# Performance work log

Measured on AMD Instinct MI355X. Metric: run time of the kernel, lower is better.

## Reference

```python
import jax, jax.numpy as jnp
import numpy as np
import math

D_MODEL = 1024
D_STATE = 64
DT_MIN, DT_MAX = 1e-3, 1e-1


def setup_inputs() -> dict:
    key = jax.random.key(0)
    ks = jax.random.split(key, 8)
    x = jax.random.normal(ks[0], (2, 4096, D_MODEL), dtype=jnp.float32)
    # in_proj / out_proj: nn.Linear default init (kaiming-uniform-ish); uniform is fine for a reference
    lim = 1.0 / math.sqrt(D_MODEL)
    Win = jax.random.uniform(ks[1], (D_MODEL, D_MODEL), minval=-lim, maxval=lim, dtype=jnp.float32)
    bin_ = jax.random.uniform(ks[2], (D_MODEL,), minval=-lim, maxval=lim, dtype=jnp.float32)
    Wout = jax.random.uniform(ks[3], (D_MODEL, D_MODEL), minval=-lim, maxval=lim, dtype=jnp.float32)
    bout = jax.random.uniform(ks[4], (D_MODEL,), minval=-lim, maxval=lim, dtype=jnp.float32)
    # HiPPO-LegS style init: A_log[d, n] = log(n + 1)
    A_log = jnp.broadcast_to(jnp.log(jnp.arange(1, D_STATE + 1, dtype=jnp.float32)), (D_MODEL, D_STATE))
    B = 0.1 * jax.random.normal(ks[5], (D_MODEL, D_STATE), dtype=jnp.float32)
    C = 0.1 * jax.random.normal(ks[6], (D_MODEL, D_STATE), dtype=jnp.float32)
    Dp = jnp.ones((D_MODEL,), dtype=jnp.float32)
    log_dt = jax.random.uniform(ks[7], (D_MODEL,), dtype=jnp.float32) * (math.log(DT_MAX) - math.log(DT_MIN)) + math.log(DT_MIN)
    dt = jnp.exp(log_dt)
    return {"x": x, "Win": Win, "bin_": bin_, "A_log": A_log, "B": B, "C": C,
            "Dp": Dp, "dt": dt, "Wout": Wout, "bout": bout}


def reference(x, Win, bin_, A_log, B, C, Dp, dt, Wout, bout):
    b, L, d = x.shape
    x = x @ Win.T + bin_                      # in_proj
    u = jnp.transpose(x, (0, 2, 1))           # [b, d, l]
    A = -jnp.exp(-A_log)                      # [d, n], negative real poles
    logdA = A * dt[:, None]                   # log(dA) since dA = exp(A*dt) > 0
    dB = B * dt[:, None]                      # [d, n]
    t = jnp.arange(L, dtype=x.dtype)
    # dA**t == exp(t * log dA): vectorized Vandermonde, replaces per-step power loop
    powers = jnp.exp(logdA[:, :, None] * t)   # [d, n, L]
    k = jnp.einsum('dn,dnl->dl', C * dB, powers)  # SSM conv kernel [d, L]
    n_fft = 2 * L
    k_f = jnp.fft.rfft(k, n=n_fft)            # [d, F]
    u_f = jnp.fft.rfft(u, n=n_fft)            # [b, d, F]
    y = jnp.fft.irfft(u_f * k_f[None], n=n_fft)[..., :L]  # causal conv
    y = y + u * Dp[:, None]                   # skip connection
    y = jnp.transpose(y, (0, 2, 1))           # [b, l, d]
    return y @ Wout.T + bout                  # out_proj
```

## Files before the change

### kernel.cpp

```cpp
#include <hip/hip_runtime.h>
#include <cstdint>
#include <cstddef>

#define D_MODEL 1024
#define D_STATE 64
#define SEQ     4096
#define BATCH   2
#define MROWS   (BATCH*SEQ)

typedef __bf16 bf16x8 __attribute__((ext_vector_type(8)));
typedef float  f32x4  __attribute__((ext_vector_type(4)));
typedef unsigned short u16;
typedef unsigned int   u32;

union BF8 { bf16x8 v; uint4 q; u16 e[8]; };

__device__ __forceinline__ u16 f2bf(float x) {
    u32 u = __float_as_uint(x);
    u32 r = u + 0x7FFFu + ((u >> 16) & 1u);
    return (u16)(r >> 16);
}
__device__ __forceinline__ float bf2f(u16 h) {
    return __uint_as_float(((u32)h) << 16);
}
__device__ __forceinline__ uint4 pack8u(const u16* e) {
    return make_uint4((u32)e[0] | ((u32)e[1] << 16), (u32)e[2] | ((u32)e[3] << 16),
                      (u32)e[4] | ((u32)e[5] << 16), (u32)e[6] | ((u32)e[7] << 16));
}

__device__ __forceinline__ void async16(const void* g, void* l) {
    __builtin_amdgcn_global_load_lds(
        (const __attribute__((address_space(1))) unsigned int*)(uintptr_t)g,
        (__attribute__((address_space(3))) unsigned int*)(uintptr_t)l,
        16, 0, 0);
}

__global__ __launch_bounds__(256) void prep_kernel(
    const float* __restrict__ x, const float* __restrict__ Win,
    const float* __restrict__ Wout,
    u16* __restrict__ Ax, u16* __restrict__ Bw1, u16* __restrict__ Bw2)
{
    const int blk = blockIdx.x, tid = threadIdx.x;
    const int k = tid * 4;
    const float* src; u16* dst; int row;
    if (blk < MROWS)                  { src = x;    dst = Ax;  row = blk; }
    else if (blk < MROWS + D_MODEL)   { src = Win;  dst = Bw1; row = blk - MROWS; }
    else                              { src = Wout; dst = Bw2; row = blk - MROWS - D_MODEL; }
    const float4 v = *reinterpret_cast<const float4*>(src + (size_t)row * D_MODEL + k);
    *reinterpret_cast<uint2*>(dst + (size_t)row * D_MODEL + k) =
        make_uint2((u32)f2bf(v.x) | ((u32)f2bf(v.y) << 16),
                   (u32)f2bf(v.z) | ((u32)f2bf(v.w) << 16));
}

template<int MODE>
__global__ __launch_bounds__(256) void gemm_bt(
    const u16* __restrict__ A, const u16* __restrict__ Bm,
    const float* __restrict__ bias, float* __restrict__ out)
{
    __shared__ u16 As[128 * 64];
    __shared__ u16 Bs[128 * 64];
    const int m0 = blockIdx.y * 128, n0 = blockIdx.x * 128;
    const int tid = threadIdx.x;
    const int wave = tid >> 6, lane = tid & 63;
    const int wm = wave >> 1, wn = wave & 1;
    const int qm = lane & 15, qk = lane >> 4;
    f32x4 acc[4][4] = {};
    for (int k0 = 0; k0 < D_MODEL; k0 += 64) {
        #pragma unroll
        for (int it = 0; it < 4; ++it) {
            const int c   = it * 256 + tid;
            const int row = c >> 3, col = (c & 7) * 8;
            const int ldsbase = (it * 256 + wave * 64) * 8;
            async16(&A[(size_t)(m0 + row) * D_MODEL + k0 + col], &As[ldsbase]);
            async16(&Bm[(size_t)(n0 + row) * D_MODEL + k0 + col], &Bs[ldsbase]);
        }
        __syncthreads();
        #pragma unroll
        for (int kk = 0; kk < 2; ++kk) {
            bf16x8 af[4], bg[4];
            #pragma unroll
            for (int i = 0; i < 4; ++i) {
                af[i] = *reinterpret_cast<const bf16x8*>(&As[(wm*64 + i*16 + qm)*64 + kk*32 + qk*8]);
                bg[i] = *reinterpret_cast<const bf16x8*>(&Bs[(wn*64 + i*16 + qm)*64 + kk*32 + qk*8]);
            }
            #pragma unroll
            for (int i = 0; i < 4; ++i)
                #pragma unroll
                for (int j = 0; j < 4; ++j)
                    acc[i][j] = __builtin_amdgcn_mfma_f32_16x16x32_bf16(af[i], bg[j], acc[i][j], 0, 0, 0);
        }
        __syncthreads();
    }
    #pragma unroll
    for (int i = 0; i < 4; ++i) {
        const int r0 = m0 + wm*64 + i*16 + qk*4;
        #pragma unroll
        for (int j = 0; j < 4; ++j) {
            const int c = n0 + wn*64 + j*16 + qm;
            const float bv = bias[c];
            if (MODE == 0) {
                #pragma unroll
                for (int reg = 0; reg < 4; ++reg)
                    out[(size_t)(r0 + reg) * D_MODEL + c] = acc[i][j][reg] + bv;
            } else {
                const int bb = r0 >> 12;
                const int l  = r0 & (SEQ - 1);
                float4 v = make_float4(acc[i][j][0] + bv, acc[i][j][1] + bv,
                                       acc[i][j][2] + bv, acc[i][j][3] + bv);
                *reinterpret_cast<float4*>(&out[((size_t)(bb * D_MODEL + c)) * SEQ + l]) = v;
            }
        }
    }
}

__global__ __launch_bounds__(64) void prep2_kernel(
    const float* __restrict__ A_log, const float* __restrict__ Bp,
    const float* __restrict__ Cp, const float* __restrict__ dtp,
    u16* __restrict__ Tg)
{
    __shared__ float P[64 * 65];
    __shared__ float k_sh[64];
    const int d = blockIdx.x, lane = threadIdx.x;
    const float dt_d  = dtp[d];
    const float logdA = -expf(-A_log[d * D_STATE + lane]) * dt_d;
    const float r     = expf(logdA);
    const float dBn   = Bp[d * D_STATE + lane] * dt_d;
    const float Cv    = Cp[d * D_STATE + lane];
    u16* tg = Tg + (size_t)d * 12288;

    {
        float p = Cv;
        for (int t = 0; t < 64; ++t) { p *= r; P[t * 65 + lane] = p; }
    }
    __syncthreads();
    {
        const int t = lane;
        for (int o = 0; o < 8; ++o) {
            u16 e[8];
            #pragma unroll
            for (int i = 0; i < 8; ++i) e[i] = f2bf(P[t * 65 + o * 8 + i]);
            *reinterpret_cast<uint4*>(&tg[8192 + t * 64 + o * 8]) = pack8u(e);
        }
    }
    __syncthreads();
    {
        float p = Cv * dBn;
        for (int m = 0; m < 64; ++m) { P[m * 65 + lane] = p; p *= r; }
    }
    __syncthreads();
    {
        float kacc = 0.f;
        for (int n = 0; n < 64; ++n) kacc += P[lane * 65 + n];
        k_sh[lane] = kacc;
    }
    __syncthreads();
    {
        const int t = lane;
        for (int o = 0; o < 8; ++o) {
            u16 e[8];
            #pragma unroll
            for (int i = 0; i < 8; ++i) {
                const int j = o * 8 + i;
                e[i] = (j <= t) ? f2bf(k_sh[t - j]) : (u16)0;
            }
            *reinterpret_cast<uint4*>(&tg[t * 64 + o * 8]) = pack8u(e);
        }
    }
    {
        for (int o = 0; o < 8; ++o) {
            float tmp[8];
            tmp[7] = expf(logdA * (float)(63 - (o * 8 + 7)));
            #pragma unroll
            for (int i = 6; i >= 0; --i) tmp[i] = tmp[i + 1] * r;
            u16 e[8];
            #pragma unroll
            for (int i = 0; i < 8; ++i) e[i] = f2bf(tmp[i]);
            *reinterpret_cast<uint4*>(&tg[4096 + lane * 64 + o * 8]) = pack8u(e);
        }
    }
}

__global__ __launch_bounds__(128) void scan2_kernel(
    float* __restrict__ ut, const float* __restrict__ A_log,
    const float* __restrict__ Bp, const float* __restrict__ dtp,
    const float* __restrict__ Dpv, const u16* __restrict__ Tg)
{
    __shared__ u16 KT_s[64 * 72];
    __shared__ u16 RA_s[64 * 72];
    __shared__ u16 P2_s[64 * 72];
    __shared__ u16 SH[2][64 * 72];
    const int d = blockIdx.x, tid = threadIdx.x;
    const int w = tid >> 6, lane = tid & 63;
    const int qm = lane & 15, qk = lane >> 4;

    const u16* tg = Tg + (size_t)d * 12288;
    #pragma unroll
    for (int it = 0; it < 12; ++it) {
        const int q = tid + it * 128;
        const int row = q >> 3, c8 = (q & 7) * 8;
        u16* dst = (row < 64)  ? &KT_s[row * 72 + c8]
                 : (row < 128) ? &RA_s[(row - 64) * 72 + c8]
                               : &P2_s[(row - 128) * 72 + c8];
        *reinterpret_cast<uint4*>(dst) =
            *reinterpret_cast<const uint4*>(&tg[row * 64 + c8]);
    }

    const float dt_d  = dtp[d];
    const float logdA = -expf(-A_log[d * D_STATE + lane]) * dt_d;
    const float dBn   = Bp[d * D_STATE + lane] * dt_d;
    const float rTn   = expf(logdA * 64.0f);
    const float Dpd   = Dpv[d];

    float* ug = ut + ((size_t)(w * D_MODEL + d)) * SEQ;

    bf16x8 Uf[4][4];
    #pragma unroll
    for (int ct = 0; ct < 4; ++ct) {
        const float* src = ug + (ct * 16 + qm) * 64;
        #pragma unroll
        for (int jb = 0; jb < 2; ++jb) {
            const float4 v0 = *reinterpret_cast<const float4*>(src + jb * 32 + qk * 8);
            const float4 v1 = *reinterpret_cast<const float4*>(src + jb * 32 + qk * 8 + 4);
            const float fv[8] = {v0.x, v0.y, v0.z, v0.w, v1.x, v1.y, v1.z, v1.w};
            BF8 hi, lo;
            #pragma unroll
            for (int i = 0; i < 8; ++i) {
                hi.e[i] = f2bf(fv[i]);
                lo.e[i] = f2bf(fv[i] - bf2f(hi.e[i]));
            }
            Uf[ct][jb]     = hi.v;
            Uf[ct][jb + 2] = lo.v;
        }
    }
    __syncthreads();

    u16* sh = SH[w];
    {
        bf16x8 Af[4][2];
        #pragma unroll
        for (int nt = 0; nt < 4; ++nt)
            #pragma unroll
            for (int jb = 0; jb < 2; ++jb)
                Af[nt][jb] = *reinterpret_cast<const bf16x8*>(
                    &RA_s[(nt * 16 + qm) * 72 + jb * 32 + qk * 8]);
        f32x4 acc[4][4] = {};
        #pragma unroll
        for (int kk = 0; kk < 4; ++kk)
            #pragma unroll
            for (int nt = 0; nt < 4; ++nt)
                #pragma unroll
                for (int ct = 0; ct < 4; ++ct)
                    acc[nt][ct] = __builtin_amdgcn_mfma_f32_16x16x32_bf16(
                        Af[nt][kk & 1], Uf[ct][kk], acc[nt][ct], 0, 0, 0);
        #pragma unroll
        for (int nt = 0; nt < 4; ++nt)
            #pragma unroll
            for (int ct = 0; ct < 4; ++ct) {
                const int c = ct * 16 + qm, nn0 = nt * 16 + qk * 4;
                uint2 pk;
                pk.x = (u32)f2bf(acc[nt][ct][0]) | ((u32)f2bf(acc[nt][ct][1]) << 16);
                pk.y = (u32)f2bf(acc[nt][ct][2]) | ((u32)f2bf(acc[nt][ct][3]) << 16);
                *reinterpret_cast<uint2*>(&sh[c * 72 + nn0]) = pk;
            }
    }
    __syncthreads();

    {
        float h = 0.f;
        for (int c = 0; c < 64; ++c) {
            const float s = bf2f(sh[c * 72 + lane]);
            sh[c * 72 + lane] = f2bf(h);
            h = rTn * h + dBn * s;
        }
    }
    __syncthreads();

    {
        bf16x8 Af[4][2];
        #pragma unroll
        for (int tt = 0; tt < 4; ++tt)
            #pragma unroll
            for (int jb = 0; jb < 2; ++jb)
                Af[tt][jb] = *reinterpret_cast<const bf16x8*>(
                    &KT_s[(tt * 16 + qm) * 72 + jb * 32 + qk * 8]);
        f32x4 acc[4][4] = {};
        #pragma unroll
        for (int kk = 0; kk < 4; ++kk)
            #pragma unroll
            for (int tt = 0; tt < 4; ++tt)
                #pragma unroll
                for (int ct = 0; ct < 4; ++ct)
                    acc[tt][ct] = __builtin_amdgcn_mfma_f32_16x16x32_bf16(
                        Af[tt][kk & 1], Uf[ct][kk], acc[tt][ct], 0, 0, 0);
        bf16x8 Pf[4][2];
        #pragma unroll
        for (int tt = 0; tt < 4; ++tt)
            #pragma unroll
            for (int kb = 0; kb < 2; ++kb)
                Pf[tt][kb] = *reinterpret_cast<const bf16x8*>(
                    &P2_s[(tt * 16 + qm) * 72 + kb * 32 + qk * 8]);
        #pragma unroll
        for (int ct = 0; ct < 4; ++ct)
            #pragma unroll
            for (int kb = 0; kb < 2; ++kb) {
                const bf16x8 Hf = *reinterpret_cast<const bf16x8*>(
                    &sh[(ct * 16 + qm) * 72 + kb * 32 + qk * 8]);
                #pragma unroll
                for (int tt = 0; tt < 4; ++tt)
                    acc[tt][ct] = __builtin_amdgcn_mfma_f32_16x16x32_bf16(
                        Pf[tt][kb], Hf, acc[tt][ct], 0, 0, 0);
            }
        #pragma unroll
        for (int tt = 0; tt < 4; ++tt)
            #pragma unroll
            for (int ct = 0; ct < 4; ++ct) {
                const int c = ct * 16 + qm, t0 = tt * 16 + qk * 4;
                float* dst = ug + c * 64 + t0;
                const float4 u4 = *reinterpret_cast<const float4*>(dst);
                float4 y;
                y.x = acc[tt][ct][0] + Dpd * u4.x;
                y.y = acc[tt][ct][1] + Dpd * u4.y;
                y.z = acc[tt][ct][2] + Dpd * u4.z;
                y.w = acc[tt][ct][3] + Dpd * u4.w;
                *reinterpret_cast<float4*>(dst) = y;
            }
    }
}

__global__ __launch_bounds__(256) void trans_kernel(
    const float* __restrict__ yt, u16* __restrict__ Ax)
{
    __shared__ float T[64 * 68];
    const int b = blockIdx.z, dx = blockIdx.y * 64, lx = blockIdx.x * 64;
    const int tid = threadIdx.x;
    const int t16 = tid >> 4, l16 = tid & 15;
    #pragma unroll
    for (int ii = 0; ii < 4; ++ii) {
        const int dd = ii * 16 + t16;
        const int ll = l16 * 4;
        float4 v = *reinterpret_cast<const float4*>(
            &yt[((size_t)(b * D_MODEL + dx + dd)) * SEQ + lx + ll]);
        *reinterpret_cast<float4*>(&T[dd * 68 + ll]) = v;
    }
    __syncthreads();
    #pragma unroll
    for (int ii = 0; ii < 4; ++ii) {
        const int ll = ii * 16 + t16;
        const int dd = l16 * 4;
        float v0 = T[(dd + 0) * 68 + ll], v1 = T[(dd + 1) * 68 + ll];
        float v2 = T[(dd + 2) * 68 + ll], v3 = T[(dd + 3) * 68 + ll];
        const size_t row = (size_t)b * SEQ + lx + ll;
        *reinterpret_cast<uint2*>(Ax + row * D_MODEL + dx + dd) =
            make_uint2((u32)f2bf(v0) | ((u32)f2bf(v1) << 16),
                       (u32)f2bf(v2) | ((u32)f2bf(v3) << 16));
    }
}

extern "C" void kernel_launch(void* const* d_in, const int* in_sizes, int n_in,
                              void* d_out, int out_size, void* d_ws, size_t ws_size,
                              hipStream_t stream) {
    const float* x     = (const float*)d_in[0];
    const float* Win   = (const float*)d_in[1];
    const float* bin   = (const float*)d_in[2];
    const float* A_log = (const float*)d_in[3];
    const float* Bp    = (const float*)d_in[4];
    const float* Cp    = (const float*)d_in[5];
    const float* Dpv   = (const float*)d_in[6];
    const float* dtp   = (const float*)d_in[7];
    const float* Wout  = (const float*)d_in[8];
    const float* bout  = (const float*)d_in[9];
    float* out = (float*)d_out;

    char* ws = (char*)d_ws;
    u16*   Ax  = (u16*)(ws);
    u16*   Tg  = (u16*)(ws);
    float* ut  = (float*)(ws + (size_t)25165824);
    u16*   Bw1 = (u16*)(ws + (size_t)58720256);
    u16*   Bw2 = (u16*)(ws + (size_t)60817408);

    prep_kernel<<<MROWS + 2 * D_MODEL, 256, 0, stream>>>(x, Win, Wout, Ax, Bw1, Bw2);
    gemm_bt<1><<<dim3(D_MODEL / 128, MROWS / 128), 256, 0, stream>>>(Ax, Bw1, bin, ut);
    prep2_kernel<<<D_MODEL, 64, 0, stream>>>(A_log, Bp, Cp, dtp, Tg);
    scan2_kernel<<<D_MODEL, 128, 0, stream>>>(ut, A_log, Bp, dtp, Dpv, Tg);
    trans_kernel<<<dim3(SEQ / 64, D_MODEL / 64, BATCH), 256, 0, stream>>>(ut, Ax);
    gemm_bt<0><<<dim3(D_MODEL / 128, MROWS / 128), 256, 0, stream>>>(Ax, Bw2, bout, out);
}
```

Baseline: 219.0 us.

## Fuse SSM kernel-table prep into scan and coalesce transposed GEMM epilogue via LDS

Removes the separate prep2 kernel. The scan kernel now computes the Toeplitz kernel table, the decay matrix and the power matrix directly in shared memory, with its two waves splitting the work, instead of reading them back from a global workspace. The first GEMM's transposed epilogue now stages each 16x64 accumulator tile through a per-wave padded LDS buffer, so each lane writes contiguous float4s along the sequence dimension instead of doing scattered float4 stores. This saves a kernel launch and global round trips, at the cost of extra LDS usage in the GEMM and redundant per-block compute in the scan.

```diff
diff --git a/kernel.cpp b/kernel.cpp
--- a/kernel.cpp
+++ b/kernel.cpp
@@ -59,6 +59,7 @@
 {
     __shared__ u16 As[128 * 64];
     __shared__ u16 Bs[128 * 64];
+    __shared__ float Tt[MODE == 1 ? 4 * 16 * 65 : 4];
     const int m0 = blockIdx.y * 128, n0 = blockIdx.x * 128;
     const int tid = threadIdx.x;
     const int wave = tid >> 6, lane = tid & 63;
@@ -91,99 +92,53 @@
         }
         __syncthreads();
     }
-    #pragma unroll
-    for (int i = 0; i < 4; ++i) {
-        const int r0 = m0 + wm*64 + i*16 + qk*4;
-        #pragma unroll
-        for (int j = 0; j < 4; ++j) {
-            const int c = n0 + wn*64 + j*16 + qm;
-            const float bv = bias[c];
-            if (MODE == 0) {
+    if (MODE == 0) {
+        #pragma unroll
+        for (int i = 0; i < 4; ++i) {
+            const int r0 = m0 + wm*64 + i*16 + qk*4;
+            #pragma unroll
+            for (int j = 0; j < 4; ++j) {
+                const int c = n0 + wn*64 + j*16 + qm;
+                const float bv = bias[c];
                 #pragma unroll
                 for (int reg = 0; reg < 4; ++reg)
                     out[(size_t)(r0 + reg) * D_MODEL + c] = acc[i][j][reg] + bv;
-            } else {
-                const int bb = r0 >> 12;
-                const int l  = r0 & (SEQ - 1);
-                float4 v = make_float4(acc[i][j][0] + bv, acc[i][j][1] + bv,
-                                       acc[i][j][2] + bv, acc[i][j][3] + bv);
-                *reinterpret_cast<float4*>(&out[((size_t)(bb * D_MODEL + c)) * SEQ + l]) = v;
-            }
-        }
-    }
-}
-
-__global__ __launch_bounds__(64) void prep2_kernel(
-    const float* __restrict__ A_log, const float* __restrict__ Bp,
-    const float* __restrict__ Cp, const float* __restrict__ dtp,
-    u16* __restrict__ Tg)
-{
-    __shared__ float P[64 * 65];
-    __shared__ float k_sh[64];
-    const int d = blockIdx.x, lane = threadIdx.x;
-    const float dt_d  = dtp[d];
-    const float logdA = -expf(-A_log[d * D_STATE + lane]) * dt_d;
-    const float r     = expf(logdA);
-    const float dBn   = Bp[d * D_STATE + lane] * dt_d;
-    const float Cv    = Cp[d * D_STATE + lane];
-    u16* tg = Tg + (size_t)d * 12288;
-
-    {
-        float p = Cv;
-        for (int t = 0; t < 64; ++t) { p *= r; P[t * 65 + lane] = p; }
-    }
-    __syncthreads();
-    {
-        const int t = lane;
-        for (int o = 0; o < 8; ++o) {
-            u16 e[8];
-            #pragma unroll
-            for (int i = 0; i < 8; ++i) e[i] = f2bf(P[t * 65 + o * 8 + i]);
-            *reinterpret_cast<uint4*>(&tg[8192 + t * 64 + o * 8]) = pack8u(e);
-        }
-    }
-    __syncthreads();
-    {
-        float p = Cv * dBn;
-        for (int m = 0; m < 64; ++m) { P[m * 65 + lane] = p; p *= r; }
-    }
-    __syncthreads();
-    {
-        float kacc = 0.f;
-        for (int n = 0; n < 64; ++n) kacc += P[lane * 65 + n];
-        k_sh[lane] = kacc;
-    }
-    __syncthreads();
-    {
-        const int t = lane;
-        for (int o = 0; o < 8; ++o) {
-            u16 e[8];
-            #pragma unroll
-            for (int i = 0; i < 8; ++i) {
-                const int j = o * 8 + i;
-                e[i] = (j <= t) ? f2bf(k_sh[t - j]) : (u16)0;
-            }
-            *reinterpret_cast<uint4*>(&tg[t * 64 + o * 8]) = pack8u(e);
-        }
-    }
-    {
-        for (int o = 0; o < 8; ++o) {
-            float tmp[8];
-            tmp[7] = expf(logdA * (float)(63 - (o * 8 + 7)));
-            #pragma unroll
-            for (int i = 6; i >= 0; --i) tmp[i] = tmp[i + 1] * r;
-            u16 e[8];
-            #pragma unroll
-            for (int i = 0; i < 8; ++i) e[i] = f2bf(tmp[i]);
-            *reinterpret_cast<uint4*>(&tg[4096 + lane * 64 + o * 8]) = pack8u(e);
+            }
+        }
+    } else {
+        float* T = &Tt[wave * 16 * 65];
+        float bvj[4];
+        #pragma unroll
+        for (int j = 0; j < 4; ++j) bvj[j] = bias[n0 + wn*64 + j*16 + qm];
+        const int dcol = n0 + wn*64 + lane;
+        #pragma unroll
+        for (int i = 0; i < 4; ++i) {
+            #pragma unroll
+            for (int j = 0; j < 4; ++j)
+                #pragma unroll
+                for (int reg = 0; reg < 4; ++reg)
+                    T[(qk*4 + reg) * 65 + j*16 + qm] = acc[i][j][reg] + bvj[j];
+            __builtin_amdgcn_wave_barrier();
+            float4 o[4];
+            #pragma unroll
+            for (int t4 = 0; t4 < 4; ++t4)
+                o[t4] = make_float4(T[(t4*4 + 0) * 65 + lane], T[(t4*4 + 1) * 65 + lane],
+                                    T[(t4*4 + 2) * 65 + lane], T[(t4*4 + 3) * 65 + lane]);
+            const int r0 = m0 + wm*64 + i*16;
+            const int bb = r0 >> 12, l0 = r0 & (SEQ - 1);
+            float* dst = &out[((size_t)(bb * D_MODEL + dcol)) * SEQ + l0];
+            #pragma unroll
+            for (int t4 = 0; t4 < 4; ++t4)
+                reinterpret_cast<float4*>(dst)[t4] = o[t4];
+            __builtin_amdgcn_wave_barrier();
         }
     }
 }
 
 __global__ __launch_bounds__(128) void scan2_kernel(
     float* __restrict__ ut, const float* __restrict__ A_log,
-    const float* __restrict__ Bp, const float* __restrict__ dtp,
-    const float* __restrict__ Dpv, const u16* __restrict__ Tg)
+    const float* __restrict__ Bp, const float* __restrict__ Cp,
+    const float* __restrict__ dtp, const float* __restrict__ Dpv)
 {
     __shared__ u16 KT_s[64 * 72];
     __shared__ u16 RA_s[64 * 72];
@@ -193,21 +148,11 @@
     const int w = tid >> 6, lane = tid & 63;
     const int qm = lane & 15, qk = lane >> 4;
 
-    const u16* tg = Tg + (size_t)d * 12288;
-    #pragma unroll
-    for (int it = 0; it < 12; ++it) {
-        const int q = tid + it * 128;
-        const int row = q >> 3, c8 = (q & 7) * 8;
-        u16* dst = (row < 64)  ? &KT_s[row * 72 + c8]
-                 : (row < 128) ? &RA_s[(row - 64) * 72 + c8]
-                               : &P2_s[(row - 128) * 72 + c8];
-        *reinterpret_cast<uint4*>(dst) =
-            *reinterpret_cast<const uint4*>(&tg[row * 64 + c8]);
-    }
-
     const float dt_d  = dtp[d];
     const float logdA = -expf(-A_log[d * D_STATE + lane]) * dt_d;
+    const float r     = expf(logdA);
     const float dBn   = Bp[d * D_STATE + lane] * dt_d;
+    const float Cv    = Cp[d * D_STATE + lane];
     const float rTn   = expf(logdA * 64.0f);
     const float Dpd   = Dpv[d];
 
@@ -230,6 +175,48 @@
             }
             Uf[ct][jb]     = hi.v;
             Uf[ct][jb + 2] = lo.v;
+        }
+    }
+
+    if (w == 1) {
+        {
+            float p = Cv;
+            for (int t = 0; t < 64; ++t) { p *= r; P2_s[t * 72 + lane] = f2bf(p); }
+        }
+        {
+            for (int o = 0; o < 8; ++o) {
+                float tmp[8];
+                tmp[7] = expf(logdA * (float)(63 - (o * 8 + 7)));
+                #pragma unroll
+                for (int i = 6; i >= 0; --i) tmp[i] = tmp[i + 1] * r;
+                u16 e[8];
+                #pragma unroll
+                for (int i = 0; i < 8; ++i) e[i] = f2bf(tmp[i]);
+                *reinterpret_cast<uint4*>(&RA_s[lane * 72 + o * 8]) = pack8u(e);
+            }
+        }
+    } else {
+        float* scr = reinterpret_cast<float*>(&SH[0][0]);
+        float* ksh = scr + 64 * 65;
+        {
+            float p = Cv * dBn;
+            for (int m = 0; m < 64; ++m) { scr[m * 65 + lane] = p; p *= r; }
+        }
+        {
+            float kacc = 0.f;
+            for (int n = 0; n < 64; ++n) kacc += scr[lane * 65 + n];
+            ksh[lane] = kacc;
+        }
+        {
+            for (int o = 0; o < 8; ++o) {
+                u16 e[8];
+                #pragma unroll
+                for (int i = 0; i < 8; ++i) {
+                    const int j = o * 8 + i;
+                    e[i] = (j <= lane) ? f2bf(ksh[lane - j]) : (u16)0;
+                }
+                *reinterpret_cast<uint4*>(&KT_s[lane * 72 + o * 8]) = pack8u(e);
+            }
         }
     }
     __syncthreads();
@@ -373,15 +360,13 @@
 
     char* ws = (char*)d_ws;
     u16*   Ax  = (u16*)(ws);
-    u16*   Tg  = (u16*)(ws);
     float* ut  = (float*)(ws + (size_t)25165824);
     u16*   Bw1 = (u16*)(ws + (size_t)58720256);
     u16*   Bw2 = (u16*)(ws + (size_t)60817408);
 
     prep_kernel<<<MROWS + 2 * D_MODEL, 256, 0, stream>>>(x, Win, Wout, Ax, Bw1, Bw2);
     gemm_bt<1><<<dim3(D_MODEL / 128, MROWS / 128), 256, 0, stream>>>(Ax, Bw1, bin, ut);
-    prep2_kernel<<<D_MODEL, 64, 0, stream>>>(A_log, Bp, Cp, dtp, Tg);
-    scan2_kernel<<<D_MODEL, 128, 0, stream>>>(ut, A_log, Bp, dtp, Dpv, Tg);
+    scan2_kernel<<<D_MODEL, 128, 0, stream>>>(ut, A_log, Bp, Cp, dtp, Dpv);
     trans_kernel<<<dim3(SEQ / 64, D_MODEL / 64, BATCH), 256, 0, stream>>>(ut, Ax);
     gemm_bt<0><<<dim3(D_MODEL / 128, MROWS / 128), 256, 0, stream>>>(Ax, Bw2, bout, out);
 }
```

After: 199.1 us. 9.1% less time.
